# Kernel optimization log

Measured on AMD Instinct MI355X. Metric: run time of the kernel, lower is better.

## Reference

```python
import jax, jax.numpy as jnp
import numpy as np

IN, H, OUT = 1536, 640, 10
BATCH = 65536
KEEP = 0.1


def setup_inputs() -> dict:
    key = jax.random.key(0)
    kx, k1, k2, k3, m1, m2, m3 = jax.random.split(key, 7)
    # torch.nn.Linear-style weights: (out_features, in_features)
    W1 = jax.random.normal(k1, (H, IN), dtype=jnp.float32) * (1.0 / np.sqrt(IN))
    W2 = jax.random.normal(k2, (H, H), dtype=jnp.float32) * (1.0 / np.sqrt(H))
    W3 = jax.random.normal(k3, (OUT, H), dtype=jnp.float32) * (1.0 / np.sqrt(H))
    return {
        "x": jax.random.normal(kx, (BATCH, IN), dtype=jnp.float32),
        "W1": W1,
        "W2": W2,
        "W3": W3,
        "mask1": jax.random.bernoulli(m1, KEEP, (H, IN)),
        "mask2": jax.random.bernoulli(m2, KEEP, (H, H)),
        "mask3": jax.random.bernoulli(m3, KEEP, (OUT, H)),
    }


def reference(x, W1, W2, W3, mask1, mask2, mask3):
    w1 = jnp.where(mask1, W1, 0.0)
    w2 = jnp.where(mask2, W2, 0.0)
    w3 = jnp.where(mask3, W3, 0.0)
    h = jax.nn.gelu(x @ w1.T, approximate=False)       # [B, 640], exact GELU like F.gelu
    h = jax.nn.gelu(h @ w2.T, approximate=False)       # [B, 640]
    return h @ w3.T                                    # [B, 10]
```

## Files before the change

### kernel.cpp

```cpp
#include <hip/hip_runtime.h>
#include <hip/hip_fp16.h>
#include <math.h>

typedef _Float16 half_t;
typedef __attribute__((ext_vector_type(8))) _Float16 f16x8;
typedef __attribute__((ext_vector_type(4))) float   f32x4;
typedef __attribute__((ext_vector_type(4))) float   float4v;

#define IN_F   1536
#define HID    640
#define OUT_F  10
#define NBATCH 65536

#define SB() __builtin_amdgcn_sched_barrier(0)


__device__ __forceinline__ void gll16(const void* g, const void* l) {
    __builtin_amdgcn_global_load_lds(
        (const __attribute__((address_space(1))) unsigned*)g,
        (__attribute__((address_space(3))) unsigned*)l, 16, 0, 0);
}

__device__ __forceinline__ float gelu_fast(float z) {
    float x  = 0.70710678118654752f * z;
    float ax = fabsf(x);
    float t  = 1.0f / (1.0f + 0.3275911f * ax);
    float p  = t * (0.254829592f +
               t * (-0.284496736f +
               t * (1.421413741f +
               t * (-1.453152027f +
               t * 1.061405429f))));
    float e  = __expf(-ax * ax);
    float er = 1.0f - p * e;
    er = (x < 0.0f) ? -er : er;
    return 0.5f * z * (1.0f + er);
}


__global__ void k_detect(const unsigned* __restrict__ m, int nDwords, int* flags) {
    int f = 0, g = 0;
    for (int i = blockIdx.x * blockDim.x + threadIdx.x; i < nDwords;
         i += gridDim.x * blockDim.x) {
        unsigned d = m[i];
        f |= (d == 0x3F800000u);
        g |= (d != 0u) & (d != 1u) & (d != 0x3F800000u);
    }
    if (f) atomicOr(&flags[0], 1);
    if (g) atomicOr(&flags[1], 1);
}

__device__ __forceinline__ bool mask_at(const void* mask, int i, int isB, int isF) {
    if (isB) return ((const unsigned char*)mask)[i] != 0;
    if (isF) return ((const float*)mask)[i] != 0.0f;
    return ((const int*)mask)[i] != 0;
}

__global__ void k_mask_all(const float* __restrict__ W1, const float* __restrict__ W2,
                           const float* __restrict__ W3,
                           const void* __restrict__ m1, const void* __restrict__ m2,
                           const void* __restrict__ m3,
                           half_t* __restrict__ W1h, half_t* __restrict__ W2h,
                           float* __restrict__ W3m, const int* __restrict__ flags) {
    const int isB = flags[1], isF = flags[0];
    const int N1 = HID * IN_F, N2 = HID * HID, N3 = OUT_F * HID;
    const int NT = N1 + N2 + N3;
    for (int i = blockIdx.x * blockDim.x + threadIdx.x; i < NT;
         i += gridDim.x * blockDim.x) {
        if (i < N1) {
            W1h[i] = mask_at(m1, i, isB, isF) ? (half_t)W1[i] : (half_t)0.0f;
        } else if (i < N1 + N2) {
            int j = i - N1;
            W2h[j] = mask_at(m2, j, isB, isF) ? (half_t)W2[j] : (half_t)0.0f;
        } else {
            int j = i - N1 - N2;
            W3m[j] = mask_at(m3, j, isB, isF) ? W3[j] : 0.0f;
        }
    }
}

template <int K, bool AF32, bool FUSE>
__global__ __launch_bounds__(512, 2) void gemm_gelu(
    const void* __restrict__ Ain, const half_t* __restrict__ Bw,
    half_t* __restrict__ Cout, const float* __restrict__ W3,
    float* __restrict__ Pout) {
    constexpr int NK     = K / 32;
    constexpr int ABYTES = AF32 ? 32768 : 16384;
    constexpr int SLAB   = ABYTES + 20480;
    constexpr int CL0    = AF32 ? 7 : 5;
    constexpr int CL1    = AF32 ? 6 : 4;
    static_assert(NK >= 4, "");
    __shared__ __align__(16) char lds[3 * SLAB];

    const int t = threadIdx.x, lane = t & 63, wid = t >> 6;
    const int wr = wid >> 2, wc = wid & 3;

    const int q       = (int)gridDim.x >> 3;
    const int logical = ((int)blockIdx.x & 7) * q + ((int)blockIdx.x >> 3);
    const int mb = logical >> 1, nbk = logical & 1;
    const long mBase = (long)mb * 256;
    const int  n0    = nbk * 320;

    const int rr = lane & 15, k8 = lane >> 4;

    int aBase0 = 0, aBase1 = 0, bBase = 0;
    {
        const int row = wr * 128 + rr;
        if constexpr (AF32) {
            aBase0 = row * 128 + (((2 * k8) ^ (row & 7)) << 4);
            aBase1 = aBase0 ^ 16;
        } else {
            const int ln = row >> 1;
            aBase0 = ln * 128 + ((((((row & 1) << 2) | k8)) ^ (ln & 7)) << 4);
        }
        const int nrow = wc * 80 + rr, lnb = nrow >> 1;
        bBase = ABYTES + lnb * 128 +
                ((((((nrow & 1) << 2) | k8)) ^ (lnb & 7)) << 4);
    }

    const float*  srcAf = nullptr;
    const half_t* srcAh = nullptr;
    if constexpr (AF32) {
        const int row = t >> 3, kq = (t & 7) ^ ((t >> 3) & 7);
        srcAf = (const float*)Ain + (mBase + row) * (long)K + kq * 4;
    } else {
        const int line = t >> 3, orig = (t & 7) ^ (line & 7);
        const int row = 2 * line + (orig >> 2), kq = orig & 3;
        srcAh = (const half_t*)Ain + (mBase + row) * (long)K + kq * 8;
    }
    const half_t* srcB;
    {
        const int line = t >> 3, orig = (t & 7) ^ (line & 7);
        const int nrow = 2 * line + (orig >> 2), kq = orig & 3;
        srcB = Bw + (size_t)(n0 + nrow) * K + kq * 8;
    }

    auto STAGE = [&](int k, int sb) {
        const size_t ko = (size_t)k * 32;
        if constexpr (AF32) {
#pragma unroll
            for (int r = 0; r < 4; ++r)
                gll16(srcAf + ko + (size_t)r * 64 * K,
                      &lds[sb + (t + r * 512) * 16]);
        } else {
#pragma unroll
            for (int r = 0; r < 2; ++r)
                gll16(srcAh + ko + (size_t)r * 128 * K,
                      &lds[sb + (t + r * 512) * 16]);
        }
#pragma unroll
        for (int r = 0; r < 2; ++r)
            gll16(srcB + ko + (size_t)r * 128 * K,
                  &lds[sb + ABYTES + (t + r * 512) * 16]);
        if (t < 256)
            gll16(srcB + ko + (size_t)2 * 128 * K,
                  &lds[sb + ABYTES + (t + 1024) * 16]);
    };

    f32x4 acc[8][5];
#pragma unroll
    for (int mf = 0; mf < 8; ++mf)
#pragma unroll
        for (int nf = 0; nf < 5; ++nf) {
            f32x4 z = {0.f, 0.f, 0.f, 0.f};
            acc[mf][nf] = z;
        }

    STAGE(0, 0); SB();
    STAGE(1, SLAB); SB();

    for (int ks = 0; ks < NK; ++ks) {
        if (ks + 1 < NK) {
            if (wid < 4) asm volatile("s_waitcnt vmcnt(%0)" :: "i"(CL0) : "memory");
            else         asm volatile("s_waitcnt vmcnt(%0)" :: "i"(CL1) : "memory");
        } else {
            asm volatile("s_waitcnt vmcnt(0)" ::: "memory");
        }
        __builtin_amdgcn_s_barrier();
        const int cb = (ks % 3) * SLAB;
        if (ks + 2 < NK) { STAGE(ks + 2, ((ks + 2) % 3) * SLAB); SB(); }

        f16x8 bv[5];
#pragma unroll
        for (int nf = 0; nf < 5; ++nf)
            bv[nf] = *(const f16x8*)(&lds[cb + bBase + nf * 1024]);
        f16x8 av[8];
        if constexpr (AF32) {
#pragma unroll
            for (int mf = 0; mf < 8; ++mf) {
                float4v alo = *(const float4v*)(&lds[cb + aBase0 + mf * 2048]);
                float4v ahi = *(const float4v*)(&lds[cb + aBase1 + mf * 2048]);
                f16x8 h;
#pragma unroll
                for (int i = 0; i < 4; ++i) {
                    h[i]     = (half_t)alo[i];
                    h[i + 4] = (half_t)ahi[i];
                }
                av[mf] = h;
            }
        } else {
#pragma unroll
            for (int mf = 0; mf < 8; ++mf)
                av[mf] = *(const f16x8*)(&lds[cb + aBase0 + mf * 1024]);
        }
#pragma unroll
        for (int mf = 0; mf < 8; ++mf)
#pragma unroll
            for (int nf = 0; nf < 5; ++nf)
                acc[mf][nf] = __builtin_amdgcn_mfma_f32_16x16x32_f16(
                    av[mf], bv[nf], acc[mf][nf], 0, 0, 0);
    }

    const int crow0 = (lane >> 4) * 4;
    const int ccol  = lane & 15;
    if constexpr (!FUSE) {
#pragma unroll
        for (int mf = 0; mf < 8; ++mf)
#pragma unroll
            for (int nf = 0; nf < 5; ++nf)
#pragma unroll
                for (int j = 0; j < 4; ++j) {
                    const long row = mBase + wr * 128 + mf * 16 + crow0 + j;
                    const int  col = n0 + wc * 80 + nf * 16 + ccol;
                    Cout[row * HID + col] = (half_t)gelu_fast(acc[mf][nf][j]);
                }
    } else {
        float w3[OUT_F][5];
#pragma unroll
        for (int o = 0; o < OUT_F; ++o)
#pragma unroll
            for (int nf = 0; nf < 5; ++nf)
                w3[o][nf] = W3[o * HID + n0 + wc * 80 + nf * 16 + ccol];
        float* slice = Pout + (size_t)(nbk * 4 + wc) * NBATCH * OUT_F;
#pragma unroll
        for (int mf = 0; mf < 8; ++mf)
#pragma unroll
            for (int j = 0; j < 4; ++j) {
                float p[OUT_F];
#pragma unroll
                for (int o = 0; o < OUT_F; ++o) p[o] = 0.f;
#pragma unroll
                for (int nf = 0; nf < 5; ++nf) {
                    const float v = gelu_fast(acc[mf][nf][j]);
#pragma unroll
                    for (int o = 0; o < OUT_F; ++o) p[o] += v * w3[o][nf];
                }
#pragma unroll
                for (int mask = 1; mask < 16; mask <<= 1)
#pragma unroll
                    for (int o = 0; o < OUT_F; ++o)
                        p[o] += __shfl_xor(p[o], mask);
                float v = 0.f;
#pragma unroll
                for (int o = 0; o < OUT_F; ++o) v = (ccol == o) ? p[o] : v;
                const long row = mBase + wr * 128 + mf * 16 + crow0 + j;
                if (ccol < OUT_F) slice[row * OUT_F + ccol] = v;
            }
    }
}

__global__ void k_final(const float* __restrict__ P, float* __restrict__ out) {
    const int n = NBATCH * OUT_F;
    for (int i = blockIdx.x * blockDim.x + threadIdx.x; i < n;
         i += gridDim.x * blockDim.x) {
        float s0 = P[i]                 + P[(size_t)1 * n + i];
        float s1 = P[(size_t)2 * n + i] + P[(size_t)3 * n + i];
        float s2 = P[(size_t)4 * n + i] + P[(size_t)5 * n + i];
        float s3 = P[(size_t)6 * n + i] + P[(size_t)7 * n + i];
        out[i] = (s0 + s1) + (s2 + s3);
    }
}


extern "C" void kernel_launch(void* const* d_in, const int* in_sizes, int n_in,
                              void* d_out, int out_size, void* d_ws, size_t ws_size,
                              hipStream_t stream) {
    const float* x  = (const float*)d_in[0];
    const float* W1 = (const float*)d_in[1];
    const float* W2 = (const float*)d_in[2];
    const float* W3 = (const float*)d_in[3];
    const void*  m1 = d_in[4];
    const void*  m2 = d_in[5];
    const void*  m3 = d_in[6];
    float* out = (float*)d_out;

    char* ws = (char*)d_ws;
    int*    flags = (int*)ws;
    half_t* W1h = (half_t*)(ws + 256);
    half_t* W2h = (half_t*)(ws + 256 + 1966080);
    float*  W3m = (float*)(ws + 256 + 1966080 + 819200);
    half_t* h1  = (half_t*)(ws + 256 + 1966080 + 819200 + 25600);
    float*  Pp  = (float*)((char*)h1 + (size_t)NBATCH * HID * 2);

    hipMemsetAsync(flags, 0, 8, stream);
    k_detect<<<64, 256, 0, stream>>>((const unsigned*)m1, 65536, flags);
    k_mask_all<<<1024, 256, 0, stream>>>(W1, W2, W3, m1, m2, m3, W1h, W2h, W3m, flags);

    gemm_gelu<IN_F, true, false><<<512, 512, 0, stream>>>(
        (const void*)x, W1h, h1, nullptr, nullptr);
    gemm_gelu<HID, false, true><<<512, 512, 0, stream>>>(
        (const void*)h1, W2h, nullptr, W3m, Pp);
    k_final<<<1024, 256, 0, stream>>>(Pp, out);
}
```

Before: 326.7 us.

## Split first GEMM into smaller-tile, double-buffered kernel with higher occupancy

Replaces the templated first-layer GEMM with a dedicated kernel that uses 128-row M tiles instead of 256, two LDS buffers instead of three, and launch bounds allowing four blocks per CU. The grid doubles to 1024 blocks. The k-loop now loads all fragments into registers, waits on LDS, and barriers before refilling the same buffer. This trades per-block reuse of the B tile for more resident waves and less LDS per block, aiming to hide the fp32 A-load latency better. The second GEMM is de-templated with unchanged logic.

```diff
diff --git a/kernel.cpp b/kernel.cpp
--- a/kernel.cpp
+++ b/kernel.cpp
@@ -78,17 +78,135 @@
     }
 }
 
-template <int K, bool AF32, bool FUSE>
-__global__ __launch_bounds__(512, 2) void gemm_gelu(
-    const void* __restrict__ Ain, const half_t* __restrict__ Bw,
-    half_t* __restrict__ Cout, const float* __restrict__ W3,
-    float* __restrict__ Pout) {
+__global__ __launch_bounds__(512, 4) void gemm1_tall(
+    const float* __restrict__ Ain, const half_t* __restrict__ Bw,
+    half_t* __restrict__ Cout) {
+    constexpr int K    = IN_F;
+    constexpr int NK   = K / 32;
+    constexpr int SLAB = 16384 + 20480;
+    __shared__ __align__(16) char lds[2 * SLAB];
+
+    const int t = threadIdx.x, lane = t & 63, wid = t >> 6;
+    const int wr = wid >> 2, wc = wid & 3;
+
+    const int q       = (int)gridDim.x >> 3;
+    const int logical = ((int)blockIdx.x & 7) * q + ((int)blockIdx.x >> 3);
+    const int mb = logical >> 1, nbk = logical & 1;
+    const long mBase = (long)mb * 128;
+    const int  n0    = nbk * 320;
+
+    const int rr = lane & 15, k8 = lane >> 4;
+
+    int aRd[4], bBase;
+    {
+#pragma unroll
+        for (int mf = 0; mf < 4; ++mf) {
+            const int row = wr * 64 + mf * 16 + rr;
+            aRd[mf] = row * 128 + (((2 * k8) ^ (row & 7)) << 4);
+        }
+        const int nrow = wc * 80 + rr, lnb = nrow >> 1;
+        bBase = 16384 + lnb * 128 +
+                ((((((nrow & 1) << 2) | k8)) ^ (lnb & 7)) << 4);
+    }
+
+    const float* srcAf;
+    {
+        const int row = t >> 3, kq = (t & 7) ^ ((t >> 3) & 7);
+        srcAf = Ain + (mBase + row) * (long)K + kq * 4;
+    }
+    const half_t* srcB;
+    {
+        const int line = t >> 3, orig = (t & 7) ^ (line & 7);
+        const int nrow = 2 * line + (orig >> 2), kq = orig & 3;
+        srcB = Bw + (size_t)(n0 + nrow) * K + kq * 8;
+    }
+
+    auto STAGE = [&](int k, int sb) {
+        const size_t ko = (size_t)k * 32;
+#pragma unroll
+        for (int r = 0; r < 2; ++r)
+            gll16(srcAf + ko + (size_t)r * 64 * K,
+                  &lds[sb + (t + r * 512) * 16]);
+#pragma unroll
+        for (int r = 0; r < 2; ++r)
+            gll16(srcB + ko + (size_t)r * 128 * K,
+                  &lds[sb + 16384 + (t + r * 512) * 16]);
+        if (t < 256)
+            gll16(srcB + ko + (size_t)2 * 128 * K,
+                  &lds[sb + 16384 + (t + 1024) * 16]);
+    };
+
+    f32x4 acc[4][5];
+#pragma unroll
+    for (int mf = 0; mf < 4; ++mf)
+#pragma unroll
+        for (int nf = 0; nf < 5; ++nf) {
+            f32x4 z = {0.f, 0.f, 0.f, 0.f};
+            acc[mf][nf] = z;
+        }
+
+    STAGE(0, 0); SB();
+    STAGE(1, SLAB); SB();
+
+    for (int ks = 0; ks < NK; ++ks) {
+        const int cb = (ks & 1) * SLAB;
+        if (ks + 1 < NK) {
+            if (wid < 4) asm volatile("s_waitcnt vmcnt(5)" ::: "memory");
+            else         asm volatile("s_waitcnt vmcnt(4)" ::: "memory");
+        } else {
+            asm volatile("s_waitcnt vmcnt(0)" ::: "memory");
+        }
+        __builtin_amdgcn_s_barrier();
+        f16x8 bv[5];
+#pragma unroll
+        for (int nf = 0; nf < 5; ++nf)
+            bv[nf] = *(const f16x8*)(&lds[cb + bBase + nf * 1024]);
+        f16x8 av[4];
+#pragma unroll
+        for (int mf = 0; mf < 4; ++mf) {
+            float4v alo = *(const float4v*)(&lds[cb + aRd[mf]]);
+            float4v ahi = *(const float4v*)(&lds[cb + (aRd[mf] ^ 16)]);
+            f16x8 h;
+#pragma unroll
+            for (int i = 0; i < 4; ++i) {
+                h[i]     = (half_t)alo[i];
+                h[i + 4] = (half_t)ahi[i];
+            }
+            av[mf] = h;
+        }
+        asm volatile("s_waitcnt lgkmcnt(0)" ::: "memory");
+        SB();
+        __builtin_amdgcn_s_barrier();
+        if (ks + 2 < NK) { STAGE(ks + 2, cb); SB(); }
+#pragma unroll
+        for (int mf = 0; mf < 4; ++mf)
+#pragma unroll
+            for (int nf = 0; nf < 5; ++nf)
+                acc[mf][nf] = __builtin_amdgcn_mfma_f32_16x16x32_f16(
+                    av[mf], bv[nf], acc[mf][nf], 0, 0, 0);
+    }
+
+    const int crow0 = (lane >> 4) * 4;
+    const int ccol  = lane & 15;
+#pragma unroll
+    for (int mf = 0; mf < 4; ++mf)
+#pragma unroll
+        for (int nf = 0; nf < 5; ++nf)
+#pragma unroll
+            for (int j = 0; j < 4; ++j) {
+                const long row = mBase + wr * 64 + mf * 16 + crow0 + j;
+                const int  col = n0 + wc * 80 + nf * 16 + ccol;
+                Cout[row * HID + col] = (half_t)gelu_fast(acc[mf][nf][j]);
+            }
+}
+
+template <int K>
+__global__ __launch_bounds__(512, 2) void gemm2_fused(
+    const half_t* __restrict__ Ain, const half_t* __restrict__ Bw,
+    const float* __restrict__ W3, float* __restrict__ Pout) {
     constexpr int NK     = K / 32;
-    constexpr int ABYTES = AF32 ? 32768 : 16384;
+    constexpr int ABYTES = 16384;
     constexpr int SLAB   = ABYTES + 20480;
-    constexpr int CL0    = AF32 ? 7 : 5;
-    constexpr int CL1    = AF32 ? 6 : 4;
-    static_assert(NK >= 4, "");
     __shared__ __align__(16) char lds[3 * SLAB];
 
     const int t = threadIdx.x, lane = t & 63, wid = t >> 6;
@@ -102,30 +220,20 @@
 
     const int rr = lane & 15, k8 = lane >> 4;
 
-    int aBase0 = 0, aBase1 = 0, bBase = 0;
-    {
-        const int row = wr * 128 + rr;
-        if constexpr (AF32) {
-            aBase0 = row * 128 + (((2 * k8) ^ (row & 7)) << 4);
-            aBase1 = aBase0 ^ 16;
-        } else {
-            const int ln = row >> 1;
-            aBase0 = ln * 128 + ((((((row & 1) << 2) | k8)) ^ (ln & 7)) << 4);
-        }
+    int aBase0 = 0, bBase = 0;
+    {
+        const int row = wr * 128 + rr, ln = row >> 1;
+        aBase0 = ln * 128 + ((((((row & 1) << 2) | k8)) ^ (ln & 7)) << 4);
         const int nrow = wc * 80 + rr, lnb = nrow >> 1;
         bBase = ABYTES + lnb * 128 +
                 ((((((nrow & 1) << 2) | k8)) ^ (lnb & 7)) << 4);
     }
 
-    const float*  srcAf = nullptr;
-    const half_t* srcAh = nullptr;
-    if constexpr (AF32) {
-        const int row = t >> 3, kq = (t & 7) ^ ((t >> 3) & 7);
-        srcAf = (const float*)Ain + (mBase + row) * (long)K + kq * 4;
-    } else {
+    const half_t* srcAh;
+    {
         const int line = t >> 3, orig = (t & 7) ^ (line & 7);
         const int row = 2 * line + (orig >> 2), kq = orig & 3;
-        srcAh = (const half_t*)Ain + (mBase + row) * (long)K + kq * 8;
+        srcAh = Ain + (mBase + row) * (long)K + kq * 8;
     }
     const half_t* srcB;
     {
@@ -136,17 +244,10 @@
 
     auto STAGE = [&](int k, int sb) {
         const size_t ko = (size_t)k * 32;
-        if constexpr (AF32) {
-#pragma unroll
-            for (int r = 0; r < 4; ++r)
-                gll16(srcAf + ko + (size_t)r * 64 * K,
-                      &lds[sb + (t + r * 512) * 16]);
-        } else {
-#pragma unroll
-            for (int r = 0; r < 2; ++r)
-                gll16(srcAh + ko + (size_t)r * 128 * K,
-                      &lds[sb + (t + r * 512) * 16]);
-        }
+#pragma unroll
+        for (int r = 0; r < 2; ++r)
+            gll16(srcAh + ko + (size_t)r * 128 * K,
+                  &lds[sb + (t + r * 512) * 16]);
 #pragma unroll
         for (int r = 0; r < 2; ++r)
             gll16(srcB + ko + (size_t)r * 128 * K,
@@ -170,8 +271,8 @@
 
     for (int ks = 0; ks < NK; ++ks) {
         if (ks + 1 < NK) {
-            if (wid < 4) asm volatile("s_waitcnt vmcnt(%0)" :: "i"(CL0) : "memory");
-            else         asm volatile("s_waitcnt vmcnt(%0)" :: "i"(CL1) : "memory");
+            if (wid < 4) asm volatile("s_waitcnt vmcnt(5)" ::: "memory");
+            else         asm volatile("s_waitcnt vmcnt(4)" ::: "memory");
         } else {
             asm volatile("s_waitcnt vmcnt(0)" ::: "memory");
         }
@@ -184,24 +285,9 @@
         for (int nf = 0; nf < 5; ++nf)
             bv[nf] = *(const f16x8*)(&lds[cb + bBase + nf * 1024]);
         f16x8 av[8];
-        if constexpr (AF32) {
-#pragma unroll
-            for (int mf = 0; mf < 8; ++mf) {
-                float4v alo = *(const float4v*)(&lds[cb + aBase0 + mf * 2048]);
-                float4v ahi = *(const float4v*)(&lds[cb + aBase1 + mf * 2048]);
-                f16x8 h;
-#pragma unroll
-                for (int i = 0; i < 4; ++i) {
-                    h[i]     = (half_t)alo[i];
-                    h[i + 4] = (half_t)ahi[i];
-                }
-                av[mf] = h;
-            }
-        } else {
-#pragma unroll
-            for (int mf = 0; mf < 8; ++mf)
-                av[mf] = *(const f16x8*)(&lds[cb + aBase0 + mf * 1024]);
-        }
+#pragma unroll
+        for (int mf = 0; mf < 8; ++mf)
+            av[mf] = *(const f16x8*)(&lds[cb + aBase0 + mf * 1024]);
 #pragma unroll
         for (int mf = 0; mf < 8; ++mf)
 #pragma unroll
@@ -212,50 +298,37 @@
 
     const int crow0 = (lane >> 4) * 4;
     const int ccol  = lane & 15;
-    if constexpr (!FUSE) {
-#pragma unroll
-        for (int mf = 0; mf < 8; ++mf)
-#pragma unroll
-            for (int nf = 0; nf < 5; ++nf)
-#pragma unroll
-                for (int j = 0; j < 4; ++j) {
-                    const long row = mBase + wr * 128 + mf * 16 + crow0 + j;
-                    const int  col = n0 + wc * 80 + nf * 16 + ccol;
-                    Cout[row * HID + col] = (half_t)gelu_fast(acc[mf][nf][j]);
-                }
-    } else {
-        float w3[OUT_F][5];
-#pragma unroll
-        for (int o = 0; o < OUT_F; ++o)
-#pragma unroll
-            for (int nf = 0; nf < 5; ++nf)
-                w3[o][nf] = W3[o * HID + n0 + wc * 80 + nf * 16 + ccol];
-        float* slice = Pout + (size_t)(nbk * 4 + wc) * NBATCH * OUT_F;
-#pragma unroll
-        for (int mf = 0; mf < 8; ++mf)
-#pragma unroll
-            for (int j = 0; j < 4; ++j) {
-                float p[OUT_F];
-#pragma unroll
-                for (int o = 0; o < OUT_F; ++o) p[o] = 0.f;
-#pragma unroll
-                for (int nf = 0; nf < 5; ++nf) {
-                    const float v = gelu_fast(acc[mf][nf][j]);
-#pragma unroll
-                    for (int o = 0; o < OUT_F; ++o) p[o] += v * w3[o][nf];
-                }
-#pragma unroll
-                for (int mask = 1; mask < 16; mask <<= 1)
-#pragma unroll
-                    for (int o = 0; o < OUT_F; ++o)
-                        p[o] += __shfl_xor(p[o], mask);
-                float v = 0.f;
-#pragma unroll
-                for (int o = 0; o < OUT_F; ++o) v = (ccol == o) ? p[o] : v;
-                const long row = mBase + wr * 128 + mf * 16 + crow0 + j;
-                if (ccol < OUT_F) slice[row * OUT_F + ccol] = v;
+    float w3[OUT_F][5];
+#pragma unroll
+    for (int o = 0; o < OUT_F; ++o)
+#pragma unroll
+        for (int nf = 0; nf < 5; ++nf)
+            w3[o][nf] = W3[o * HID + n0 + wc * 80 + nf * 16 + ccol];
+    float* slice = Pout + (size_t)(nbk * 4 + wc) * NBATCH * OUT_F;
+#pragma unroll
+    for (int mf = 0; mf < 8; ++mf)
+#pragma unroll
+        for (int j = 0; j < 4; ++j) {
+            float p[OUT_F];
+#pragma unroll
+            for (int o = 0; o < OUT_F; ++o) p[o] = 0.f;
+#pragma unroll
+            for (int nf = 0; nf < 5; ++nf) {
+                const float v = gelu_fast(acc[mf][nf][j]);
+#pragma unroll
+                for (int o = 0; o < OUT_F; ++o) p[o] += v * w3[o][nf];
             }
-    }
+#pragma unroll
+            for (int mask = 1; mask < 16; mask <<= 1)
+#pragma unroll
+                for (int o = 0; o < OUT_F; ++o)
+                    p[o] += __shfl_xor(p[o], mask);
+            float v = 0.f;
+#pragma unroll
+            for (int o = 0; o < OUT_F; ++o) v = (ccol == o) ? p[o] : v;
+            const long row = mBase + wr * 128 + mf * 16 + crow0 + j;
+            if (ccol < OUT_F) slice[row * OUT_F + ccol] = v;
+        }
 }
 
 __global__ void k_final(const float* __restrict__ P, float* __restrict__ out) {
@@ -295,9 +368,7 @@
     k_detect<<<64, 256, 0, stream>>>((const unsigned*)m1, 65536, flags);
     k_mask_all<<<1024, 256, 0, stream>>>(W1, W2, W3, m1, m2, m3, W1h, W2h, W3m, flags);
 
-    gemm_gelu<IN_F, true, false><<<512, 512, 0, stream>>>(
-        (const void*)x, W1h, h1, nullptr, nullptr);
-    gemm_gelu<HID, false, true><<<512, 512, 0, stream>>>(
-        (const void*)h1, W2h, nullptr, W3m, Pp);
+    gemm1_tall<<<1024, 512, 0, stream>>>(x, W1h, h1);
+    gemm2_fused<HID><<<512, 512, 0, stream>>>(h1, W2h, W3m, Pp);
     k_final<<<1024, 256, 0, stream>>>(Pp, out);
 }
```

Result: slower. 985.4 us (+201.6%).
